# Performance work log

Hardware: AMD Instinct MI355X
Metric: run time of the kernel (lower is better)

Reference implementation:

```python
import jax, jax.numpy as jnp
import numpy as np

N_PRO = 100000
N_LIG = 100000
E = 500000
H = 128
CE = 18


def _lin_params(key, out_dim, in_dim, scale=0.02):
    kw, kb = jax.random.split(key)
    W = jax.random.normal(kw, (out_dim, in_dim), jnp.float32) * scale
    b = jax.random.normal(kb, (out_dim,), jnp.float32) * scale
    return W, b


def setup_inputs() -> dict:
    key = jax.random.key(0)
    ks = jax.random.split(key, 16)
    inp = {}
    inp['pro_x'] = jax.random.normal(ks[0], (N_PRO, H), jnp.float32)
    inp['lig_x'] = jax.random.normal(ks[1], (N_LIG, H), jnp.float32)
    pi = jax.random.randint(ks[2], (E,), 0, N_PRO)
    li = jax.random.randint(ks[3], (E,), 0, N_LIG)
    inp['cross_ei'] = jnp.stack([pi, li]).astype(jnp.int64)
    inp['cross_ea'] = jax.random.normal(ks[4], (E, CE), jnp.float32)
    inp['Wq_pro'], inp['bq_pro'] = _lin_params(ks[5], H, H)
    inp['Wk_lig'], inp['bk_lig'] = _lin_params(ks[6], H, H)
    inp['Wv_lig'], inp['bv_lig'] = _lin_params(ks[7], H, H)
    inp['Wq_lig'], inp['bq_lig'] = _lin_params(ks[8], H, H)
    inp['Wk_pro'], inp['bk_pro'] = _lin_params(ks[9], H, H)
    inp['Wv_pro'], inp['bv_pro'] = _lin_params(ks[10], H, H)
    inp['We_bias'] = jax.random.normal(ks[11], (CE,), jnp.float32) * 0.02  # Linear(CE,1,bias=False) weight
    inp['Wo_pro'], inp['bo_pro'] = _lin_params(ks[12], H, H)
    inp['Wo_lig'], inp['bo_lig'] = _lin_params(ks[13], H, H)
    inp['g_pro'] = jnp.ones((H,), jnp.float32)
    inp['be_pro'] = jnp.zeros((H,), jnp.float32)
    inp['g_lig'] = jnp.ones((H,), jnp.float32)
    inp['be_lig'] = jnp.zeros((H,), jnp.float32)
    return inp


def _layernorm(x, g, b, eps=1e-5):
    mu = jnp.mean(x, -1, keepdims=True)
    var = jnp.var(x, -1, keepdims=True)
    return (x - mu) * jax.lax.rsqrt(var + eps) * g + b


def _lin(x, W, b):
    return x @ W.T + b


def _attend(Q_src, K_tgt, V_tgt, bias, tgt_idx, n_tgt, scale):
    # per-edge score -> edge softmax over target nodes -> weighted scatter-add
    scores = jnp.sum(Q_src * K_tgt, -1) * scale + bias          # [E]
    scores = scores - jnp.max(scores)                            # global max, as in torch code
    exp_s = jnp.exp(scores)
    denom = jax.ops.segment_sum(exp_s, tgt_idx, num_segments=n_tgt)
    w = exp_s / (denom[tgt_idx] + 1e-8)                          # [E]
    return jax.ops.segment_sum(w[:, None] * V_tgt, tgt_idx, num_segments=n_tgt)  # [n_tgt, H]


def reference(pro_x, lig_x, cross_ei, cross_ea,
              Wq_pro, bq_pro, Wk_lig, bk_lig, Wv_lig, bv_lig,
              Wq_lig, bq_lig, Wk_pro, bk_pro, Wv_pro, bv_pro,
              We_bias, Wo_pro, bo_pro, Wo_lig, bo_lig,
              g_pro, be_pro, g_lig, be_lig):
    pi = cross_ei[0]
    li = cross_ei[1]
    h = pro_x.shape[1]
    scale = h ** (-0.5)
    bias = cross_ea @ We_bias                                    # [E]

    # protein <- ligand
    Qp = _lin(pro_x, Wq_pro, bq_pro)[pi]
    Kl = _lin(lig_x, Wk_lig, bk_lig)[li]
    Vl = _lin(lig_x, Wv_lig, bv_lig)[li]
    pro_upd = _attend(Qp, Kl, Vl, bias, pi, pro_x.shape[0], scale)
    pro_new = _layernorm(pro_x + _lin(pro_upd, Wo_pro, bo_pro), g_pro, be_pro)

    # ligand <- protein
    Ql = _lin(lig_x, Wq_lig, bq_lig)[li]
    Kp = _lin(pro_x, Wk_pro, bk_pro)[pi]
    Vp = _lin(pro_x, Wv_pro, bv_pro)[pi]
    lig_upd = _attend(Ql, Kp, Vp, bias, li, lig_x.shape[0], scale)
    lig_new = _layernorm(lig_x + _lin(lig_upd, Wo_lig, bo_lig), g_lig, be_lig)

    return (pro_new, lig_new)
```

## Files before the change

### kernel.cpp

```cpp
#include <hip/hip_runtime.h>
#include <float.h>
#include <math.h>


typedef __bf16 bf16x8 __attribute__((ext_vector_type(8)));
typedef float  f32x4  __attribute__((ext_vector_type(4)));
typedef float  f32x2  __attribute__((ext_vector_type(2)));
typedef unsigned int u32x2 __attribute__((ext_vector_type(2)));

__device__ __forceinline__ bf16x8 cvt8(const float* p) {
    f32x4 lo = *reinterpret_cast<const f32x4*>(p);
    f32x4 hi = *reinterpret_cast<const f32x4*>(p + 4);
    bf16x8 r;
    r[0] = (__bf16)lo[0]; r[1] = (__bf16)lo[1]; r[2] = (__bf16)lo[2]; r[3] = (__bf16)lo[3];
    r[4] = (__bf16)hi[0]; r[5] = (__bf16)hi[1]; r[6] = (__bf16)hi[2]; r[7] = (__bf16)hi[3];
    return r;
}

__device__ __forceinline__ u32x2 pack_fp8x8(const float* v) {
    int w0 = __builtin_amdgcn_cvt_pk_fp8_f32(v[0], v[1], 0, false);
    w0 = __builtin_amdgcn_cvt_pk_fp8_f32(v[2], v[3], w0, true);
    int w1 = __builtin_amdgcn_cvt_pk_fp8_f32(v[4], v[5], 0, false);
    w1 = __builtin_amdgcn_cvt_pk_fp8_f32(v[6], v[7], w1, true);
    u32x2 r; r[0] = (unsigned)w0; r[1] = (unsigned)w1;
    return r;
}

__device__ __forceinline__ void unpack_fp8x8(u32x2 p, float* out) {
    f32x2 t0 = __builtin_amdgcn_cvt_pk_f32_fp8((int)p[0], false);
    f32x2 t1 = __builtin_amdgcn_cvt_pk_f32_fp8((int)p[0], true);
    f32x2 t2 = __builtin_amdgcn_cvt_pk_f32_fp8((int)p[1], false);
    f32x2 t3 = __builtin_amdgcn_cvt_pk_f32_fp8((int)p[1], true);
    out[0] = t0[0]; out[1] = t0[1]; out[2] = t1[0]; out[3] = t1[1];
    out[4] = t2[0]; out[5] = t2[1]; out[6] = t3[0]; out[7] = t3[1];
}

__device__ __forceinline__ void stage_w(const __bf16* __restrict__ Ws, char* wlds, int tid) {
#pragma unroll
    for (int it = 0; it < 8; ++it) {
        int idx = it * 2048 + tid * 8;
        int byteoff = idx * 2;
        int row = byteoff >> 8;
        *reinterpret_cast<bf16x8*>(wlds + (byteoff ^ ((row & 7) << 4)))
            = *reinterpret_cast<const bf16x8*>(Ws + idx);
    }
}
__device__ __forceinline__ bf16x8 read_w(const char* wlds, int l15, int lg, int ni, int ks) {
    int row = ni * 16 + l15;
    int off = (row * 256 + ks * 64 + lg * 16) ^ ((row & 7) << 4);
    return *reinterpret_cast<const bf16x8*>(wlds + off);
}

__global__ __launch_bounds__(256) void cvt_bias_count(
    const float* w0, const float* w1, const float* w2, const float* w3,
    const float* w4, const float* w5, const float* w6, const float* w7,
    __bf16* __restrict__ dst,
    const float* __restrict__ ea, const float* __restrict__ We,
    const int* __restrict__ pi, const int* __restrict__ li,
    float* __restrict__ bias, int* __restrict__ counts,
    unsigned* __restrict__ ranks, int Np, int E, int CE)
{
    if (blockIdx.x < 64) {
        const float* srcs[8] = {w0, w1, w2, w3, w4, w5, w6, w7};
        int t = blockIdx.x * 256 + threadIdx.x;
        int mat = t >> 11;
        int base = (t & 2047) * 8;
        const float* s = srcs[mat];
        bool perm = (mat == 3) || (mat == 7);
        __bf16* d = dst + (size_t)mat * 16384;
#pragma unroll
        for (int u = 0; u < 8; ++u) {
            int idx = base + u;
            int row = idx >> 7, c = idx & 127;
            int pos = perm ? ((c & 15) * 8 + (c >> 4)) : c;
            d[row * 128 + pos] = (__bf16)s[idx];
        }
        return;
    }
    int e = (blockIdx.x - 64) * 256 + threadIdx.x;
    if (e >= E) return;
    const float2* row = reinterpret_cast<const float2*>(ea + (size_t)e * CE);
    float acc = 0.f;
    int h = CE >> 1;
    for (int c = 0; c < h; ++c) {
        float2 v = row[c];
        acc += v.x * We[2 * c] + v.y * We[2 * c + 1];
    }
    if (CE & 1) acc += ea[(size_t)e * CE + CE - 1] * We[CE - 1];
    bias[e] = acc;
    int r0 = atomicAdd(&counts[pi[e]], 1);
    int r1 = atomicAdd(&counts[Np + li[e]], 1);
    ranks[e] = (unsigned)(r0 & 0xFFFF) | ((unsigned)r1 << 16);
}

__global__ __launch_bounds__(256) void scan1(
    const int* __restrict__ counts, int* __restrict__ offs,
    int* __restrict__ bsums, int N)
{
    int idx = blockIdx.x * 256 + threadIdx.x;
    int v = (idx < N) ? counts[idx] : 0;
    int lane = threadIdx.x & 63, w = threadIdx.x >> 6;
    int x = v;
#pragma unroll
    for (int d = 1; d < 64; d <<= 1) {
        int y = __shfl_up(x, d);
        if (lane >= d) x += y;
    }
    __shared__ int wsum[4];
    if (lane == 63) wsum[w] = x;
    __syncthreads();
    int add = 0;
    for (int i = 0; i < w; ++i) add += wsum[i];
    x += add;
    if (idx < N) offs[idx] = x - v;
    if (threadIdx.x == 255) bsums[blockIdx.x] = x;
}

__global__ __launch_bounds__(256) void scan3(
    int* __restrict__ offs, const int* __restrict__ bsums, int N, int total)
{
    int b = blockIdx.x, t = threadIdx.x;
    int s = 0;
    for (int i = t; i < b; i += 256) s += bsums[i];
#pragma unroll
    for (int d = 1; d < 64; d <<= 1) s += __shfl_xor(s, d);
    __shared__ int ws_[4];
    if ((t & 63) == 0) ws_[t >> 6] = s;
    __syncthreads();
    int pre = ws_[0] + ws_[1] + ws_[2] + ws_[3];
    int idx = b * 256 + t;
    if (idx < N) offs[idx] += pre;
    if (idx == 0) offs[N] = total;
}

__global__ __launch_bounds__(256) void fill2(
    const int* __restrict__ pi, const int* __restrict__ li,
    const float* __restrict__ bias, const unsigned* __restrict__ ranks,
    const int* __restrict__ offs, unsigned* __restrict__ elist, int Np, int E)
{
    int e = blockIdx.x * 256 + threadIdx.x;
    if (e >= E) return;
    int p = pi[e], l = li[e];
    unsigned rk = ranks[e];
    int w = __builtin_amdgcn_cvt_pk_fp8_f32(bias[e], 0.f, 0, false);
    unsigned b8 = (unsigned)w & 0xFFu;
    elist[offs[p] + (rk & 0xFFFFu)]  = ((unsigned)l << 8) | b8;
    elist[offs[Np + l] + (rk >> 16)] = ((unsigned)p << 8) | b8;
}

__global__ __launch_bounds__(256) void proj3both(
    const float* __restrict__ Xp, const float* __restrict__ Xl,
    const __bf16* __restrict__ W16,
    const float* __restrict__ bq_p, const float* __restrict__ bk_p, const float* __restrict__ bv_p,
    const float* __restrict__ bq_l, const float* __restrict__ bk_l, const float* __restrict__ bv_l,
    char* __restrict__ QKVp, char* __restrict__ QKVl,
    int Np, int Nl, int nbp)
{
    __shared__ char wlds[32768];
    int bid = blockIdx.x;
    int tid = threadIdx.x;
    int lane = tid & 63, wv = tid >> 6;
    int l15 = lane & 15, lg = lane >> 4;

    const float* A; const __bf16* Wms[3];
    const float* bsels[3]; char* QKV; int M, wrow;
    if (bid < nbp) {
        A = Xp; M = Np; wrow = bid * 64 + wv * 16;
        Wms[0] = W16 + 0 * 16384; Wms[1] = W16 + 5 * 16384; Wms[2] = W16 + 6 * 16384;
        bsels[0] = bq_p; bsels[1] = bk_p; bsels[2] = bv_p; QKV = QKVp;
    } else {
        A = Xl; M = Nl; wrow = (bid - nbp) * 64 + wv * 16;
        Wms[0] = W16 + 4 * 16384; Wms[1] = W16 + 1 * 16384; Wms[2] = W16 + 2 * 16384;
        bsels[0] = bq_l; bsels[1] = bk_l; bsels[2] = bv_l; QKV = QKVl;
    }
    int r0 = wrow + l15; if (r0 > M - 1) r0 = M - 1;
    const float* Arow0 = A + (size_t)r0 * 128 + lg * 8;

    bf16x8 a0[4];
#pragma unroll
    for (int ks = 0; ks < 4; ++ks) a0[ks] = cvt8(Arow0 + ks * 32);

#pragma unroll
    for (int mat = 0; mat < 3; ++mat) {
        __syncthreads();
        stage_w(Wms[mat], wlds, tid);
        __syncthreads();

        f32x4 acc[8] = {};
#pragma unroll
        for (int ks = 0; ks < 4; ++ks) {
#pragma unroll
            for (int ni = 0; ni < 8; ++ni)
                acc[ni] = __builtin_amdgcn_mfma_f32_16x16x32_bf16(
                    a0[ks], read_w(wlds, l15, lg, ni, ks), acc[ni], 0, 0, 0);
        }
        float bc[8];
#pragma unroll
        for (int ni = 0; ni < 8; ++ni) bc[ni] = bsels[mat][ni * 16 + l15];
#pragma unroll
        for (int r = 0; r < 4; ++r) {
            int row = wrow + lg * 4 + r;
            if (row < M) {
                float v[8];
#pragma unroll
                for (int ni = 0; ni < 8; ++ni) v[ni] = acc[ni][r] + bc[ni];
                char* rowb = QKV + (size_t)row * 512;
                if (mat == 0) {
                    bf16x8 o;
#pragma unroll
                    for (int ni = 0; ni < 8; ++ni) o[ni] = (__bf16)v[ni];
                    *reinterpret_cast<bf16x8*>(rowb + l15 * 16) = o;
                } else {
                    *reinterpret_cast<u32x2*>(rowb + 256 + (mat - 1) * 128 + l15 * 8)
                        = pack_fp8x8(v);
                }
            }
        }
    }
}

__global__ __launch_bounds__(256) void attend(
    const char* __restrict__ QKVp, const char* __restrict__ QKVl,
    const unsigned* __restrict__ elist, const int* __restrict__ offs,
    __bf16* __restrict__ upd_pro, __bf16* __restrict__ upd_lig,
    int Np, int Ntot, float scale)
{
    int node = blockIdx.x * 16 + (threadIdx.x >> 4);
    if (node >= Ntot) return;
    int l = threadIdx.x & 15;
    const char* Qrow; const char* KV; __bf16* upd;
    if (node < Np) {
        Qrow = QKVp + (size_t)node * 512; KV = QKVl;
        upd = upd_pro + (size_t)node * 128;
    } else {
        int n = node - Np;
        Qrow = QKVl + (size_t)n * 512; KV = QKVp;
        upd = upd_lig + (size_t)n * 128;
    }
    bf16x8 qv = *reinterpret_cast<const bf16x8*>(Qrow + l * 16);
    float q[8];
#pragma unroll
    for (int j = 0; j < 8; ++j) q[j] = (float)qv[j];

    int beg = offs[node], end = offs[node + 1];
    float d = 0.f;
    float acc[8] = {};
    int i = beg;
    for (; i + 1 < end; i += 2) {
        unsigned rec0 = elist[i], rec1 = elist[i + 1];
        const char* row0 = KV + (size_t)(rec0 >> 8) * 512;
        const char* row1 = KV + (size_t)(rec1 >> 8) * 512;
        u32x2 kk0 = *reinterpret_cast<const u32x2*>(row0 + 256 + l * 8);
        u32x2 vp0 = *reinterpret_cast<const u32x2*>(row0 + 384 + l * 8);
        u32x2 kk1 = *reinterpret_cast<const u32x2*>(row1 + 256 + l * 8);
        u32x2 vp1 = *reinterpret_cast<const u32x2*>(row1 + 384 + l * 8);
        float kf0[8], vf0[8], kf1[8], vf1[8];
        unpack_fp8x8(kk0, kf0); unpack_fp8x8(vp0, vf0);
        unpack_fp8x8(kk1, kf1); unpack_fp8x8(vp1, vf1);
        float dot0 = 0.f, dot1 = 0.f;
#pragma unroll
        for (int j = 0; j < 8; ++j) { dot0 += q[j] * kf0[j]; dot1 += q[j] * kf1[j]; }
#pragma unroll
        for (int t = 1; t < 16; t <<= 1) {
            dot0 += __shfl_xor(dot0, t, 16);
            dot1 += __shfl_xor(dot1, t, 16);
        }
        f32x2 b0 = __builtin_amdgcn_cvt_pk_f32_fp8((int)(rec0 & 0xFFu), false);
        f32x2 b1 = __builtin_amdgcn_cvt_pk_f32_fp8((int)(rec1 & 0xFFu), false);
        float p0 = __expf(fminf(dot0 * scale + b0[0], 60.f));
        float p1 = __expf(fminf(dot1 * scale + b1[0], 60.f));
        d += p0 + p1;
#pragma unroll
        for (int j = 0; j < 8; ++j) acc[j] += p0 * vf0[j] + p1 * vf1[j];
    }
    if (i < end) {
        unsigned rec = elist[i];
        const char* row = KV + (size_t)(rec >> 8) * 512;
        u32x2 kk = *reinterpret_cast<const u32x2*>(row + 256 + l * 8);
        u32x2 vp = *reinterpret_cast<const u32x2*>(row + 384 + l * 8);
        float kf[8], vf[8];
        unpack_fp8x8(kk, kf); unpack_fp8x8(vp, vf);
        float dot = 0.f;
#pragma unroll
        for (int j = 0; j < 8; ++j) dot += q[j] * kf[j];
#pragma unroll
        for (int t = 1; t < 16; t <<= 1) dot += __shfl_xor(dot, t, 16);
        f32x2 bt = __builtin_amdgcn_cvt_pk_f32_fp8((int)(rec & 0xFFu), false);
        float p = __expf(fminf(dot * scale + bt[0], 60.f));
        d += p;
#pragma unroll
        for (int j = 0; j < 8; ++j) acc[j] += p * vf[j];
    }
    float inv = 1.f / (d + 1e-8f);
    bf16x8 o;
#pragma unroll
    for (int j = 0; j < 8; ++j) o[j] = (__bf16)(acc[j] * inv);
    *reinterpret_cast<bf16x8*>(upd + l * 8) = o;
}

__global__ __launch_bounds__(256) void gemm_ln_both(
    const __bf16* __restrict__ upd_pro, const __bf16* __restrict__ upd_lig,
    const float* __restrict__ Xp, const float* __restrict__ Xl,
    const __bf16* __restrict__ W16,
    const float* __restrict__ bo_p, const float* __restrict__ g_p, const float* __restrict__ be_p,
    const float* __restrict__ bo_l, const float* __restrict__ g_l, const float* __restrict__ be_l,
    float* __restrict__ out_pro, float* __restrict__ out_lig,
    int Np, int Nl, int nbp)
{
    __shared__ char wlds[32768];
    int bid = blockIdx.x;
    int tid = threadIdx.x;
    int lane = tid & 63, wv = tid >> 6;
    int l15 = lane & 15, lg = lane >> 4;

    const __bf16* A; const float* X; const __bf16* Wo;
    const float *b, *g, *be_; float* C; int M, wrow;
    if (bid < nbp) {
        A = upd_pro; X = Xp; Wo = W16 + 3 * 16384;
        b = bo_p; g = g_p; be_ = be_p; C = out_pro; M = Np; wrow = bid * 64 + wv * 16;
    } else {
        A = upd_lig; X = Xl; Wo = W16 + 7 * 16384;
        b = bo_l; g = g_l; be_ = be_l; C = out_lig; M = Nl; wrow = (bid - nbp) * 64 + wv * 16;
    }
    stage_w(Wo, wlds, tid);

    int r0 = wrow + l15; if (r0 > M - 1) r0 = M - 1;
    const __bf16* Arow0 = A + (size_t)r0 * 128 + lg * 8;
    bf16x8 a0[4];
#pragma unroll
    for (int ks = 0; ks < 4; ++ks)
        a0[ks] = *reinterpret_cast<const bf16x8*>(Arow0 + ks * 32);
    __syncthreads();

    f32x4 acc[8] = {};
#pragma unroll
    for (int ks = 0; ks < 4; ++ks) {
#pragma unroll
        for (int ni = 0; ni < 8; ++ni)
            acc[ni] = __builtin_amdgcn_mfma_f32_16x16x32_bf16(
                a0[ks], read_w(wlds, l15, lg, ni, ks), acc[ni], 0, 0, 0);
    }

    float bcol[8], gcol[8], becol[8];
#pragma unroll
    for (int ni = 0; ni < 8; ++ni) {
        bcol[ni]  = b[ni * 16 + l15];
        gcol[ni]  = g[ni * 16 + l15];
        becol[ni] = be_[ni * 16 + l15];
    }

#pragma unroll
    for (int r = 0; r < 4; ++r) {
        int row = wrow + lg * 4 + r;
        bool ok = row < M;
        int rowc = ok ? row : M - 1;
        float v[8];
#pragma unroll
        for (int ni = 0; ni < 8; ++ni) v[ni] = acc[ni][r] + bcol[ni];
        const float* Xr = X + (size_t)rowc * 128 + l15;
        float s1 = 0.f, s2 = 0.f;
#pragma unroll
        for (int ni = 0; ni < 8; ++ni) {
            v[ni] += Xr[ni * 16];
            s1 += v[ni]; s2 += v[ni] * v[ni];
        }
#pragma unroll
        for (int d = 1; d < 16; d <<= 1) {
            s1 += __shfl_xor(s1, d);
            s2 += __shfl_xor(s2, d);
        }
        float mu = s1 * 0.0078125f;
        float var = s2 * 0.0078125f - mu * mu;
        float rstd = rsqrtf(var + 1e-5f);
        if (ok) {
            float* Cr = C + (size_t)row * 128 + l15;
#pragma unroll
            for (int ni = 0; ni < 8; ++ni)
                Cr[ni * 16] = (v[ni] - mu) * rstd * gcol[ni] + becol[ni];
        }
    }
}

static inline int cdiv(int a, int b) { return (a + b - 1) / b; }

extern "C" void kernel_launch(void* const* d_in, const int* in_sizes, int n_in,
                              void* d_out, int out_size, void* d_ws, size_t ws_size,
                              hipStream_t stream)
{
    const float* pro_x  = (const float*)d_in[0];
    const float* lig_x  = (const float*)d_in[1];
    const int*   ei     = (const int*)d_in[2];
    const float* ea     = (const float*)d_in[3];
    const float* Wq_pro = (const float*)d_in[4];  const float* bq_pro = (const float*)d_in[5];
    const float* Wk_lig = (const float*)d_in[6];  const float* bk_lig = (const float*)d_in[7];
    const float* Wv_lig = (const float*)d_in[8];  const float* bv_lig = (const float*)d_in[9];
    const float* Wq_lig = (const float*)d_in[10]; const float* bq_lig = (const float*)d_in[11];
    const float* Wk_pro = (const float*)d_in[12]; const float* bk_pro = (const float*)d_in[13];
    const float* Wv_pro = (const float*)d_in[14]; const float* bv_pro = (const float*)d_in[15];
    const float* We     = (const float*)d_in[16];
    const float* Wo_pro = (const float*)d_in[17]; const float* bo_pro = (const float*)d_in[18];
    const float* Wo_lig = (const float*)d_in[19]; const float* bo_lig = (const float*)d_in[20];
    const float* g_pro  = (const float*)d_in[21]; const float* be_pro = (const float*)d_in[22];
    const float* g_lig  = (const float*)d_in[23]; const float* be_lig = (const float*)d_in[24];

    const int Np = in_sizes[0] / 128;
    const int Nl = in_sizes[1] / 128;
    const int E  = in_sizes[2] / 2;
    const int CE = in_sizes[3] / E;
    const int Nmax = Np > Nl ? Np : Nl;
    const int Ntot = Np + Nl;
    const int* pi = ei;
    const int* li = ei + E;

    float* out_pro = (float*)d_out;
    float* out_lig = out_pro + (size_t)Np * 128;

    float* ws = (float*)d_ws;
    size_t o = 0;
    char* QKVp = (char*)(ws + o); o += (size_t)Nmax * 128;
    char* QKVl = (char*)(ws + o); o += (size_t)Nmax * 128;
    float* bias = ws + o;   o += (size_t)E;
    unsigned* ranks = (unsigned*)(ws + o); o += (size_t)E;
    unsigned* elist = (unsigned*)(ws + o); o += 2 * (size_t)E;
    int* counts = (int*)(ws + o); o += (size_t)Ntot + 8;
    int* offs   = (int*)(ws + o); o += (size_t)Ntot + 8;
    int* bsums  = (int*)(ws + o); o += 4096;
    __bf16* W16 = (__bf16*)(ws + o); o += 8 * 16384 / 2;
    __bf16* upd = (__bf16*)(ws + o); o += (size_t)Ntot * 64;
    __bf16* upd_pro = upd;
    __bf16* upd_lig = upd + (size_t)Np * 128;
    (void)ws_size; (void)n_in; (void)out_size;

    const float scale = 1.0f / sqrtf(128.0f);
    const int nEB = cdiv(E, 256);

    (void)hipMemsetAsync(counts, 0, (size_t)(Ntot + 1) * sizeof(int), stream);
    cvt_bias_count<<<64 + nEB, 256, 0, stream>>>(
        Wq_pro, Wk_lig, Wv_lig, Wo_pro, Wq_lig, Wk_pro, Wv_pro, Wo_lig, W16,
        ea, We, pi, li, bias, counts, ranks, Np, E, CE);

    const int nb1 = cdiv(Ntot, 256);
    scan1<<<nb1, 256, 0, stream>>>(counts, offs, bsums, Ntot);
    scan3<<<nb1, 256, 0, stream>>>(offs, bsums, Ntot, 2 * E);
    fill2<<<nEB, 256, 0, stream>>>(pi, li, bias, ranks, offs, elist, Np, E);

    const int nbp = cdiv(Np, 64), nbl = cdiv(Nl, 64);
    proj3both<<<nbp + nbl, 256, 0, stream>>>(pro_x, lig_x, W16,
        bq_pro, bk_pro, bv_pro, bq_lig, bk_lig, bv_lig,
        QKVp, QKVl, Np, Nl, nbp);

    attend<<<cdiv(Ntot, 16), 256, 0, stream>>>(QKVp, QKVl, elist, offs,
        upd_pro, upd_lig, Np, Ntot, scale);

    gemm_ln_both<<<nbp + nbl, 256, 0, stream>>>(upd_pro, upd_lig,
        pro_x, lig_x, W16, bo_pro, g_pro, be_pro, bo_lig, g_lig, be_lig,
        out_pro, out_lig, Np, Nl, nbp);
}
```

Measured before the change: 249.3 us.

## Make QKV projection persistent with atomic tile scheduler and resident weights

Turns the QKV projection into a persistent kernel: 256 blocks of 512 threads stage the Q and K weight matrices into 64KB LDS once, then waves pull 16-row tiles from global atomic counters. A second pass restages the V weights and repeats the loop. This removes the per-block weight restaging and the three syncs per tile of the old grid, but each input row is now read and converted twice and every tile costs an atomic. The counters are zeroed by widening the existing memset.

```diff
diff --git a/kernel.cpp b/kernel.cpp
--- a/kernel.cpp
+++ b/kernel.cpp
@@ -39,6 +39,16 @@
 #pragma unroll
     for (int it = 0; it < 8; ++it) {
         int idx = it * 2048 + tid * 8;
+        int byteoff = idx * 2;
+        int row = byteoff >> 8;
+        *reinterpret_cast<bf16x8*>(wlds + (byteoff ^ ((row & 7) << 4)))
+            = *reinterpret_cast<const bf16x8*>(Ws + idx);
+    }
+}
+__device__ __forceinline__ void stage_w512(const __bf16* __restrict__ Ws, char* wlds, int tid) {
+#pragma unroll
+    for (int it = 0; it < 4; ++it) {
+        int idx = it * 4096 + tid * 8;
         int byteoff = idx * 2;
         int row = byteoff >> 8;
         *reinterpret_cast<bf16x8*>(wlds + (byteoff ^ ((row & 7) << 4)))
@@ -148,43 +158,106 @@
     elist[offs[Np + l] + (rk >> 16)] = ((unsigned)p << 8) | b8;
 }
 
-__global__ __launch_bounds__(256) void proj3both(
+__global__ __launch_bounds__(512) void proj3both(
     const float* __restrict__ Xp, const float* __restrict__ Xl,
     const __bf16* __restrict__ W16,
     const float* __restrict__ bq_p, const float* __restrict__ bk_p, const float* __restrict__ bv_p,
     const float* __restrict__ bq_l, const float* __restrict__ bk_l, const float* __restrict__ bv_l,
     char* __restrict__ QKVp, char* __restrict__ QKVl,
-    int Np, int Nl, int nbp)
-{
-    __shared__ char wlds[32768];
-    int bid = blockIdx.x;
+    int Np, int Nl, int NBP, int* __restrict__ tctr)
+{
+    __shared__ char wlds[65536];
     int tid = threadIdx.x;
-    int lane = tid & 63, wv = tid >> 6;
-    int l15 = lane & 15, lg = lane >> 4;
-
-    const float* A; const __bf16* Wms[3];
-    const float* bsels[3]; char* QKV; int M, wrow;
-    if (bid < nbp) {
-        A = Xp; M = Np; wrow = bid * 64 + wv * 16;
-        Wms[0] = W16 + 0 * 16384; Wms[1] = W16 + 5 * 16384; Wms[2] = W16 + 6 * 16384;
-        bsels[0] = bq_p; bsels[1] = bk_p; bsels[2] = bv_p; QKV = QKVp;
+    int lane = tid & 63;
+    int l15 = lane & 15, lg = (lane >> 4) & 3;
+
+    const float* A; const __bf16 *Wm0, *Wm1, *Wm2;
+    const float *bQ, *bK, *bV; char* QKV; int M; int* c1; int* c2;
+    if ((int)blockIdx.x < NBP) {
+        A = Xp; M = Np;
+        Wm0 = W16 + 0 * 16384; Wm1 = W16 + 5 * 16384; Wm2 = W16 + 6 * 16384;
+        bQ = bq_p; bK = bk_p; bV = bv_p; QKV = QKVp;
+        c1 = tctr + 0; c2 = tctr + 1;
     } else {
-        A = Xl; M = Nl; wrow = (bid - nbp) * 64 + wv * 16;
-        Wms[0] = W16 + 4 * 16384; Wms[1] = W16 + 1 * 16384; Wms[2] = W16 + 2 * 16384;
-        bsels[0] = bq_l; bsels[1] = bk_l; bsels[2] = bv_l; QKV = QKVl;
-    }
-    int r0 = wrow + l15; if (r0 > M - 1) r0 = M - 1;
-    const float* Arow0 = A + (size_t)r0 * 128 + lg * 8;
-
-    bf16x8 a0[4];
-#pragma unroll
-    for (int ks = 0; ks < 4; ++ks) a0[ks] = cvt8(Arow0 + ks * 32);
-
-#pragma unroll
-    for (int mat = 0; mat < 3; ++mat) {
-        __syncthreads();
-        stage_w(Wms[mat], wlds, tid);
-        __syncthreads();
+        A = Xl; M = Nl;
+        Wm0 = W16 + 4 * 16384; Wm1 = W16 + 1 * 16384; Wm2 = W16 + 2 * 16384;
+        bQ = bq_l; bK = bk_l; bV = bv_l; QKV = QKVl;
+        c1 = tctr + 2; c2 = tctr + 3;
+    }
+    const int nt = (M + 15) >> 4;
+
+    stage_w512(Wm0, wlds, tid);
+    stage_w512(Wm1, wlds + 32768, tid);
+    __syncthreads();
+
+    float bQc[8], bKc[8], bVc[8];
+#pragma unroll
+    for (int ni = 0; ni < 8; ++ni) {
+        bQc[ni] = bQ[ni * 16 + l15];
+        bKc[ni] = bK[ni * 16 + l15];
+        bVc[ni] = bV[ni * 16 + l15];
+    }
+
+    for (;;) {
+        int t = 0;
+        if (lane == 0) t = atomicAdd(c1, 1);
+        t = __shfl(t, 0);
+        if (t >= nt) break;
+        int wrow = t << 4;
+        int r0 = wrow + l15; if (r0 > M - 1) r0 = M - 1;
+        const float* Arow0 = A + (size_t)r0 * 128 + lg * 8;
+        bf16x8 a0[4];
+#pragma unroll
+        for (int ks = 0; ks < 4; ++ks) a0[ks] = cvt8(Arow0 + ks * 32);
+
+#pragma unroll
+        for (int mat = 0; mat < 2; ++mat) {
+            const char* wl = wlds + mat * 32768;
+            f32x4 acc[8] = {};
+#pragma unroll
+            for (int ks = 0; ks < 4; ++ks) {
+#pragma unroll
+                for (int ni = 0; ni < 8; ++ni)
+                    acc[ni] = __builtin_amdgcn_mfma_f32_16x16x32_bf16(
+                        a0[ks], read_w(wl, l15, lg, ni, ks), acc[ni], 0, 0, 0);
+            }
+#pragma unroll
+            for (int r = 0; r < 4; ++r) {
+                int row = wrow + lg * 4 + r;
+                if (row < M) {
+                    float v[8];
+#pragma unroll
+                    for (int ni = 0; ni < 8; ++ni)
+                        v[ni] = acc[ni][r] + (mat == 0 ? bQc[ni] : bKc[ni]);
+                    char* rowb = QKV + (size_t)row * 512;
+                    if (mat == 0) {
+                        bf16x8 o;
+#pragma unroll
+                        for (int ni = 0; ni < 8; ++ni) o[ni] = (__bf16)v[ni];
+                        *reinterpret_cast<bf16x8*>(rowb + l15 * 16) = o;
+                    } else {
+                        *reinterpret_cast<u32x2*>(rowb + 256 + l15 * 8) = pack_fp8x8(v);
+                    }
+                }
+            }
+        }
+    }
+
+    __syncthreads();
+    stage_w512(Wm2, wlds, tid);
+    __syncthreads();
+
+    for (;;) {
+        int t = 0;
+        if (lane == 0) t = atomicAdd(c2, 1);
+        t = __shfl(t, 0);
+        if (t >= nt) break;
+        int wrow = t << 4;
+        int r0 = wrow + l15; if (r0 > M - 1) r0 = M - 1;
+        const float* Arow0 = A + (size_t)r0 * 128 + lg * 8;
+        bf16x8 a0[4];
+#pragma unroll
+        for (int ks = 0; ks < 4; ++ks) a0[ks] = cvt8(Arow0 + ks * 32);
 
         f32x4 acc[8] = {};
 #pragma unroll
@@ -194,26 +267,15 @@
                 acc[ni] = __builtin_amdgcn_mfma_f32_16x16x32_bf16(
                     a0[ks], read_w(wlds, l15, lg, ni, ks), acc[ni], 0, 0, 0);
         }
-        float bc[8];
-#pragma unroll
-        for (int ni = 0; ni < 8; ++ni) bc[ni] = bsels[mat][ni * 16 + l15];
 #pragma unroll
         for (int r = 0; r < 4; ++r) {
             int row = wrow + lg * 4 + r;
             if (row < M) {
                 float v[8];
 #pragma unroll
-                for (int ni = 0; ni < 8; ++ni) v[ni] = acc[ni][r] + bc[ni];
-                char* rowb = QKV + (size_t)row * 512;
-                if (mat == 0) {
-                    bf16x8 o;
-#pragma unroll
-                    for (int ni = 0; ni < 8; ++ni) o[ni] = (__bf16)v[ni];
-                    *reinterpret_cast<bf16x8*>(rowb + l15 * 16) = o;
-                } else {
-                    *reinterpret_cast<u32x2*>(rowb + 256 + (mat - 1) * 128 + l15 * 8)
-                        = pack_fp8x8(v);
-                }
+                for (int ni = 0; ni < 8; ++ni) v[ni] = acc[ni][r] + bVc[ni];
+                *reinterpret_cast<u32x2*>(QKV + (size_t)row * 512 + 384 + l15 * 8)
+                    = pack_fp8x8(v);
             }
         }
     }
@@ -429,12 +491,13 @@
     __bf16* upd = (__bf16*)(ws + o); o += (size_t)Ntot * 64;
     __bf16* upd_pro = upd;
     __bf16* upd_lig = upd + (size_t)Np * 128;
+    int* tctr = counts + Ntot + 1;
     (void)ws_size; (void)n_in; (void)out_size;
 
     const float scale = 1.0f / sqrtf(128.0f);
     const int nEB = cdiv(E, 256);
 
-    (void)hipMemsetAsync(counts, 0, (size_t)(Ntot + 1) * sizeof(int), stream);
+    (void)hipMemsetAsync(counts, 0, (size_t)(Ntot + 8) * sizeof(int), stream);
     cvt_bias_count<<<64 + nEB, 256, 0, stream>>>(
         Wq_pro, Wk_lig, Wv_lig, Wo_pro, Wq_lig, Wk_pro, Wv_pro, Wo_lig, W16,
         ea, We, pi, li, bias, counts, ranks, Np, E, CE);
@@ -444,14 +507,15 @@
     scan3<<<nb1, 256, 0, stream>>>(offs, bsums, Ntot, 2 * E);
     fill2<<<nEB, 256, 0, stream>>>(pi, li, bias, ranks, offs, elist, Np, E);
 
-    const int nbp = cdiv(Np, 64), nbl = cdiv(Nl, 64);
-    proj3both<<<nbp + nbl, 256, 0, stream>>>(pro_x, lig_x, W16,
+    const int NBP = 128, NBL = 128;
+    proj3both<<<NBP + NBL, 512, 0, stream>>>(pro_x, lig_x, W16,
         bq_pro, bk_pro, bv_pro, bq_lig, bk_lig, bv_lig,
-        QKVp, QKVl, Np, Nl, nbp);
+        QKVp, QKVl, Np, Nl, NBP, tctr);
 
     attend<<<cdiv(Ntot, 16), 256, 0, stream>>>(QKVp, QKVl, elist, offs,
         upd_pro, upd_lig, Np, Ntot, scale);
 
+    const int nbp = cdiv(Np, 64), nbl = cdiv(Nl, 64);
     gemm_ln_both<<<nbp + nbl, 256, 0, stream>>>(upd_pro, upd_lig,
         pro_x, lig_x, W16, bo_pro, g_pro, be_pro, bo_lig, g_lig, be_lig,
         out_pro, out_lig, Np, Nl, nbp);
```

Result: slower. 534.8 us (+114.6%).

## Use fp8 MFMA for QKV projections and stage all three weights once

Applied to the files above, without the earlier changes.

Switches the QKV projection kernel from bf16 to fp8 MFMA: the Q/K/V weights and input rows are quantized to fp8, and all three weight matrices are staged into padded LDS up front instead of being restaged between matrices behind two barriers. Weight conversion is reorganized so only the output projections stay in bf16. This aims to cut LDS traffic and synchronization and double MFMA throughput, but it raises LDS use per block (lowering occupancy) and loses precision on the inputs and weights.

```diff
diff --git a/kernel.cpp b/kernel.cpp
--- a/kernel.cpp
+++ b/kernel.cpp
@@ -35,6 +35,10 @@
     out[4] = t2[0]; out[5] = t2[1]; out[6] = t3[0]; out[7] = t3[1];
 }
 
+__device__ __forceinline__ long pack_fp8x8_l(const float* v) {
+    return __builtin_bit_cast(long, pack_fp8x8(v));
+}
+
 __device__ __forceinline__ void stage_w(const __bf16* __restrict__ Ws, char* wlds, int tid) {
 #pragma unroll
     for (int it = 0; it < 8; ++it) {
@@ -51,28 +55,55 @@
     return *reinterpret_cast<const bf16x8*>(wlds + off);
 }
 
+__device__ __forceinline__ void stage_w8(const unsigned char* __restrict__ W8m, char* dst, int tid) {
+#pragma unroll
+    for (int it = 0; it < 8; ++it) {
+        int idx = it * 2048 + tid * 8;
+        int row = idx >> 7, col = idx & 127;
+        *reinterpret_cast<u32x2*>(dst + row * 136 + col)
+            = *reinterpret_cast<const u32x2*>(W8m + idx);
+    }
+}
+__device__ __forceinline__ long read_w8(const char* base, int l15, int lg, int ni, int ks) {
+    int off = (ni * 16 + l15) * 136 + ks * 32 + lg * 8;
+    return *reinterpret_cast<const long*>(base + off);
+}
+
 __global__ __launch_bounds__(256) void cvt_bias_count(
-    const float* w0, const float* w1, const float* w2, const float* w3,
-    const float* w4, const float* w5, const float* w6, const float* w7,
-    __bf16* __restrict__ dst,
+    const float* wq_p, const float* wk_p, const float* wv_p,
+    const float* wq_l, const float* wk_l, const float* wv_l,
+    const float* wo_p, const float* wo_l,
+    unsigned char* __restrict__ W8, __bf16* __restrict__ W16,
     const float* __restrict__ ea, const float* __restrict__ We,
     const int* __restrict__ pi, const int* __restrict__ li,
     float* __restrict__ bias, int* __restrict__ counts,
     unsigned* __restrict__ ranks, int Np, int E, int CE)
 {
+    if (blockIdx.x < 48) {
+        const float* srcs[6] = {wq_p, wk_p, wv_p, wq_l, wk_l, wv_l};
+        int mat = blockIdx.x >> 3;
+        int t = (blockIdx.x & 7) * 256 + threadIdx.x;
+        int off = t * 8;
+        float v[8];
+        f32x4 lo = *reinterpret_cast<const f32x4*>(srcs[mat] + off);
+        f32x4 hi = *reinterpret_cast<const f32x4*>(srcs[mat] + off + 4);
+        v[0] = lo[0]; v[1] = lo[1]; v[2] = lo[2]; v[3] = lo[3];
+        v[4] = hi[0]; v[5] = hi[1]; v[6] = hi[2]; v[7] = hi[3];
+        *reinterpret_cast<u32x2*>(W8 + (size_t)mat * 16384 + off) = pack_fp8x8(v);
+        return;
+    }
     if (blockIdx.x < 64) {
-        const float* srcs[8] = {w0, w1, w2, w3, w4, w5, w6, w7};
-        int t = blockIdx.x * 256 + threadIdx.x;
-        int mat = t >> 11;
-        int base = (t & 2047) * 8;
+        const float* srcs[2] = {wo_p, wo_l};
+        int mat = (blockIdx.x - 48) >> 3;
+        int t = ((blockIdx.x - 48) & 7) * 256 + threadIdx.x;
+        int base = t * 8;
         const float* s = srcs[mat];
-        bool perm = (mat == 3) || (mat == 7);
-        __bf16* d = dst + (size_t)mat * 16384;
+        __bf16* d = W16 + (size_t)mat * 16384;
 #pragma unroll
         for (int u = 0; u < 8; ++u) {
             int idx = base + u;
             int row = idx >> 7, c = idx & 127;
-            int pos = perm ? ((c & 15) * 8 + (c >> 4)) : c;
+            int pos = (c & 15) * 8 + (c >> 4);
             d[row * 128 + pos] = (__bf16)s[idx];
         }
         return;
@@ -150,49 +181,59 @@
 
 __global__ __launch_bounds__(256) void proj3both(
     const float* __restrict__ Xp, const float* __restrict__ Xl,
-    const __bf16* __restrict__ W16,
+    const unsigned char* __restrict__ W8,
     const float* __restrict__ bq_p, const float* __restrict__ bk_p, const float* __restrict__ bv_p,
     const float* __restrict__ bq_l, const float* __restrict__ bk_l, const float* __restrict__ bv_l,
     char* __restrict__ QKVp, char* __restrict__ QKVl,
     int Np, int Nl, int nbp)
 {
-    __shared__ char wlds[32768];
+    __shared__ char wlds[52224];
     int bid = blockIdx.x;
     int tid = threadIdx.x;
     int lane = tid & 63, wv = tid >> 6;
     int l15 = lane & 15, lg = lane >> 4;
 
-    const float* A; const __bf16* Wms[3];
+    const float* A; const unsigned char* Wb8;
     const float* bsels[3]; char* QKV; int M, wrow;
     if (bid < nbp) {
         A = Xp; M = Np; wrow = bid * 64 + wv * 16;
-        Wms[0] = W16 + 0 * 16384; Wms[1] = W16 + 5 * 16384; Wms[2] = W16 + 6 * 16384;
+        Wb8 = W8;
         bsels[0] = bq_p; bsels[1] = bk_p; bsels[2] = bv_p; QKV = QKVp;
     } else {
         A = Xl; M = Nl; wrow = (bid - nbp) * 64 + wv * 16;
-        Wms[0] = W16 + 4 * 16384; Wms[1] = W16 + 1 * 16384; Wms[2] = W16 + 2 * 16384;
+        Wb8 = W8 + 3 * 16384;
         bsels[0] = bq_l; bsels[1] = bk_l; bsels[2] = bv_l; QKV = QKVl;
     }
+
+    stage_w8(Wb8 + 0 * 16384, wlds + 0 * 17408, tid);
+    stage_w8(Wb8 + 1 * 16384, wlds + 1 * 17408, tid);
+    stage_w8(Wb8 + 2 * 16384, wlds + 2 * 17408, tid);
+
     int r0 = wrow + l15; if (r0 > M - 1) r0 = M - 1;
     const float* Arow0 = A + (size_t)r0 * 128 + lg * 8;
 
-    bf16x8 a0[4];
-#pragma unroll
-    for (int ks = 0; ks < 4; ++ks) a0[ks] = cvt8(Arow0 + ks * 32);
+    long a8[4];
+#pragma unroll
+    for (int ks = 0; ks < 4; ++ks) {
+        float v[8];
+        f32x4 lo = *reinterpret_cast<const f32x4*>(Arow0 + ks * 32);
+        f32x4 hi = *reinterpret_cast<const f32x4*>(Arow0 + ks * 32 + 4);
+        v[0] = lo[0]; v[1] = lo[1]; v[2] = lo[2]; v[3] = lo[3];
+        v[4] = hi[0]; v[5] = hi[1]; v[6] = hi[2]; v[7] = hi[3];
+        a8[ks] = pack_fp8x8_l(v);
+    }
+    __syncthreads();
 
 #pragma unroll
     for (int mat = 0; mat < 3; ++mat) {
-        __syncthreads();
-        stage_w(Wms[mat], wlds, tid);
-        __syncthreads();
-
+        const char* wl = wlds + mat * 17408;
         f32x4 acc[8] = {};
 #pragma unroll
         for (int ks = 0; ks < 4; ++ks) {
 #pragma unroll
             for (int ni = 0; ni < 8; ++ni)
-                acc[ni] = __builtin_amdgcn_mfma_f32_16x16x32_bf16(
-                    a0[ks], read_w(wlds, l15, lg, ni, ks), acc[ni], 0, 0, 0);
+                acc[ni] = __builtin_amdgcn_mfma_f32_16x16x32_fp8_fp8(
+                    a8[ks], read_w8(wl, l15, lg, ni, ks), acc[ni], 0, 0, 0);
         }
         float bc[8];
 #pragma unroll
@@ -316,10 +357,10 @@
     const __bf16* A; const float* X; const __bf16* Wo;
     const float *b, *g, *be_; float* C; int M, wrow;
     if (bid < nbp) {
-        A = upd_pro; X = Xp; Wo = W16 + 3 * 16384;
+        A = upd_pro; X = Xp; Wo = W16;
         b = bo_p; g = g_p; be_ = be_p; C = out_pro; M = Np; wrow = bid * 64 + wv * 16;
     } else {
-        A = upd_lig; X = Xl; Wo = W16 + 7 * 16384;
+        A = upd_lig; X = Xl; Wo = W16 + 16384;
         b = bo_l; g = g_l; be_ = be_l; C = out_lig; M = Nl; wrow = (bid - nbp) * 64 + wv * 16;
     }
     stage_w(Wo, wlds, tid);
@@ -425,7 +466,8 @@
     int* counts = (int*)(ws + o); o += (size_t)Ntot + 8;
     int* offs   = (int*)(ws + o); o += (size_t)Ntot + 8;
     int* bsums  = (int*)(ws + o); o += 4096;
-    __bf16* W16 = (__bf16*)(ws + o); o += 8 * 16384 / 2;
+    unsigned char* W8 = (unsigned char*)(ws + o); o += 6 * 16384 / 4;
+    __bf16* W16 = (__bf16*)(ws + o); o += 2 * 16384 / 2;
     __bf16* upd = (__bf16*)(ws + o); o += (size_t)Ntot * 64;
     __bf16* upd_pro = upd;
     __bf16* upd_lig = upd + (size_t)Np * 128;
@@ -434,10 +476,10 @@
     const float scale = 1.0f / sqrtf(128.0f);
     const int nEB = cdiv(E, 256);
 
-    (void)hipMemsetAsync(counts, 0, (size_t)(Ntot + 1) * sizeof(int), stream);
+    (void)hipMemsetAsync(counts, 0, (size_t)(Ntot + 8) * sizeof(int), stream);
     cvt_bias_count<<<64 + nEB, 256, 0, stream>>>(
-        Wq_pro, Wk_lig, Wv_lig, Wo_pro, Wq_lig, Wk_pro, Wv_pro, Wo_lig, W16,
-        ea, We, pi, li, bias, counts, ranks, Np, E, CE);
+        Wq_pro, Wk_pro, Wv_pro, Wq_lig, Wk_lig, Wv_lig, Wo_pro, Wo_lig,
+        W8, W16, ea, We, pi, li, bias, counts, ranks, Np, E, CE);
 
     const int nb1 = cdiv(Ntot, 256);
     scan1<<<nb1, 256, 0, stream>>>(counts, offs, bsums, Ntot);
@@ -445,7 +487,7 @@
     fill2<<<nEB, 256, 0, stream>>>(pi, li, bias, ranks, offs, elist, Np, E);
 
     const int nbp = cdiv(Np, 64), nbl = cdiv(Nl, 64);
-    proj3both<<<nbp + nbl, 256, 0, stream>>>(pro_x, lig_x, W16,
+    proj3both<<<nbp + nbl, 256, 0, stream>>>(pro_x, lig_x, W8,
         bq_pro, bk_pro, bv_pro, bq_lig, bk_lig, bv_lig,
         QKVp, QKVl, Np, Nl, nbp);
 
```

After: 242.2 us. 2.8% less time.
